# Kernel tuning notes

Measured on AMD Instinct MI355X. Metric: run time of the kernel, lower is better.

Reference implementation:

```python
import jax, jax.numpy as jnp
import numpy as np

NUM_R = 725
NUM_T = 180
EPS = 1e-6


def _hough(img):
    """Discrete Hough transform: params[r, t] = sum of img along line
    x*cos(theta_t) + y*sin(theta_t) = rho_r.
    Gather form: sweep along the longer axis of the line (x-sweep when
    |sin|>=|cos|, else y-sweep) so every line is sampled densely.
    """
    W, H = img.shape  # assume square (W == H) so both sweeps share length
    diag = jnp.sqrt(jnp.asarray(W * W + H * H, dtype=img.dtype))
    thetas = jnp.arange(NUM_T, dtype=img.dtype) * (jnp.pi / NUM_T)      # [T]
    rhos = jnp.linspace(-diag, diag, NUM_R, dtype=img.dtype)            # [R]
    cos_t = jnp.cos(thetas)                                             # [T]
    sin_t = jnp.sin(thetas)                                             # [T]
    n = jnp.arange(W)                                                   # sweep coord [N]
    nf = n.astype(img.dtype)

    rho_b = rhos[:, None, None]          # [R,1,1]
    cos_b = cos_t[None, :, None]         # [1,T,1]
    sin_b = sin_t[None, :, None]
    n_b = nf[None, None, :]              # [1,1,N]

    # --- x-sweep: x = n, y = (rho - x*cos) / sin ---
    sin_safe = jnp.where(jnp.abs(sin_b) < EPS, jnp.asarray(1.0, img.dtype), sin_b)
    y_f = (rho_b - n_b * cos_b) / sin_safe
    y_i = jnp.round(y_f).astype(jnp.int32)                              # [R,T,N]
    valid_x = (y_i >= 0) & (y_i < H)
    vals_x = jnp.where(valid_x,
                       img[n[None, None, :], jnp.clip(y_i, 0, H - 1)],
                       jnp.asarray(0.0, img.dtype))

    # --- y-sweep: y = n, x = (rho - y*sin) / cos ---
    cos_safe = jnp.where(jnp.abs(cos_b) < EPS, jnp.asarray(1.0, img.dtype), cos_b)
    x_f = (rho_b - n_b * sin_b) / cos_safe
    x_i = jnp.round(x_f).astype(jnp.int32)
    valid_y = (x_i >= 0) & (x_i < W)
    vals_y = jnp.where(valid_y,
                       img[jnp.clip(x_i, 0, W - 1), n[None, None, :]],
                       jnp.asarray(0.0, img.dtype))

    use_x = (jnp.abs(sin_t) >= jnp.abs(cos_t))[None, :, None]           # [1,T,1]
    vals = jnp.where(use_x, vals_x, vals_y)
    return jnp.sum(vals, axis=-1)                                        # [R,T]


def setup_inputs() -> dict:
    key = jax.random.key(0)
    img = jax.random.uniform(key, (512, 512), dtype=jnp.float32)
    return {"img": img}


def reference(img):
    return _hough(img)
```

## Files before the change

kernel.cpp:

```cpp
#include <hip/hip_runtime.h>
#include <math.h>

#define W 512
#define H 512
#define NUM_R 725
#define NUM_T 180

__global__ __launch_bounds__(256) void transpose_k(const float* __restrict__ in,
                                                   float* __restrict__ out) {
    __shared__ float tile[32][33];
    const int bx = blockIdx.x * 32, by = blockIdx.y * 32;
    const int tx = threadIdx.x, ty = threadIdx.y;
#pragma unroll
    for (int j = 0; j < 32; j += 8)
        tile[ty + j][tx] = in[(size_t)(by + ty + j) * W + (bx + tx)];
    __syncthreads();
#pragma unroll
    for (int j = 0; j < 32; j += 8)
        out[(size_t)(bx + ty + j) * H + (by + tx)] = tile[tx][ty + j];
}

__global__ __launch_bounds__(256) void hough_k(const float* __restrict__ img,
                                               const float* __restrict__ imgT,
                                               float* __restrict__ out,
                                               int hasT) {
    const int t = blockIdx.x;
    const int r = blockIdx.y * 256 + threadIdx.x;
    const int rc = (r < NUM_R) ? r : (NUM_R - 1);

    const double theta = (double)t * (M_PI / 180.0);
    const double s = sin(theta);
    const double c = cos(theta);
    const bool use_x = fabs(s) >= fabs(c);
    double dd = use_x ? s : c;
    if (fabs(dd) < 1e-6) dd = 1.0;
    const double a   = use_x ? c : s;
    const double inv = 1.0 / dd;
    const double nk2 = -(a * inv);

    const double diag = sqrt(524288.0);
    const double step = (2.0 * diag) / 724.0;
    double rho = (double)rc * step - diag;
    if (rc == NUM_R - 1) rho = diag;

    const double SCALE = 1099511627776.0;
    const long long NK2q = (long long)rint(nk2 * SCALE);
    long long Y = (long long)rint(rho * inv * SCALE) + (1ll << 39);

    float acc = 0.f;

    if (use_x || hasT) {
        const float* __restrict__ base = use_x ? img : imgT;
#pragma unroll 8
        for (int n = 0; n < W; ++n) {
            const int y = (int)(Y >> 40);
            Y += NK2q;
            const int yc = min(max(y, 0), W - 1);
            const float v = base[n * W + yc];
            acc += ((unsigned)y < (unsigned)W) ? v : 0.f;
        }
    } else {
#pragma unroll 4
        for (int n = 0; n < W; ++n) {
            const int y = (int)(Y >> 40);
            Y += NK2q;
            const int yc = min(max(y, 0), W - 1);
            const float v = img[yc * W + n];
            acc += ((unsigned)y < (unsigned)W) ? v : 0.f;
        }
    }

    if (r < NUM_R) out[(size_t)r * NUM_T + t] = acc;
}

extern "C" void kernel_launch(void* const* d_in, const int* in_sizes, int n_in,
                              void* d_out, int out_size, void* d_ws, size_t ws_size,
                              hipStream_t stream) {
    const float* img = (const float*)d_in[0];
    float* out = (float*)d_out;

    const int hasT = (ws_size >= (size_t)W * H * sizeof(float)) ? 1 : 0;
    float* imgT = (float*)d_ws;
    if (hasT) {
        transpose_k<<<dim3(16, 16), dim3(32, 8), 0, stream>>>(img, imgT);
    }

    hough_k<<<dim3(NUM_T, (NUM_R + 255) / 256), dim3(256), 0, stream>>>(
        img, hasT ? imgT : img, out, hasT);
}
```

Baseline: 85.60 us.

## Replace gather Hough with pixel-scatter into shared-memory rho accumulators

Switches from a per-(rho,theta) gather along lines to a scatter formulation. Each block takes one theta and a chunk of image rows, reads pixels coalesced as float2, computes each pixel's rho bin in fixed point, and adds the value into shared-memory accumulators when it lies within the rounding window. The block partials are then atomically added into an output zeroed with memset. This removes the transpose pass and the uncoalesced gathers, but adds shared atomics, a global atomic reduction and an extra memset, and it may not reproduce the reference's rounding and bin membership exactly.

```diff
diff --git a/kernel.cpp b/kernel.cpp
--- a/kernel.cpp
+++ b/kernel.cpp
@@ -5,72 +5,69 @@
 #define H 512
 #define NUM_R 725
 #define NUM_T 180
+#define RCHUNK 64
 
-__global__ __launch_bounds__(256) void transpose_k(const float* __restrict__ in,
-                                                   float* __restrict__ out) {
-    __shared__ float tile[32][33];
-    const int bx = blockIdx.x * 32, by = blockIdx.y * 32;
-    const int tx = threadIdx.x, ty = threadIdx.y;
-#pragma unroll
-    for (int j = 0; j < 32; j += 8)
-        tile[ty + j][tx] = in[(size_t)(by + ty + j) * W + (bx + tx)];
+__global__ __launch_bounds__(256) void hough_scatter_k(const float* __restrict__ img,
+                                                       float* __restrict__ out) {
+    const int t   = blockIdx.x;
+    const int n0  = blockIdx.y * RCHUNK;
+    const int tid = threadIdx.x;
+
+    __shared__ float racc[768];
+
+    racc[tid] = 0.f;
+    racc[tid + 256] = 0.f;
+    racc[tid + 512] = 0.f;
     __syncthreads();
-#pragma unroll
-    for (int j = 0; j < 32; j += 8)
-        out[(size_t)(bx + ty + j) * H + (by + tx)] = tile[tx][ty + j];
-}
-
-__global__ __launch_bounds__(256) void hough_k(const float* __restrict__ img,
-                                               const float* __restrict__ imgT,
-                                               float* __restrict__ out,
-                                               int hasT) {
-    const int t = blockIdx.x;
-    const int r = blockIdx.y * 256 + threadIdx.x;
-    const int rc = (r < NUM_R) ? r : (NUM_R - 1);
 
     const double theta = (double)t * (M_PI / 180.0);
     const double s = sin(theta);
     const double c = cos(theta);
-    const bool use_x = fabs(s) >= fabs(c);
-    double dd = use_x ? s : c;
-    if (fabs(dd) < 1e-6) dd = 1.0;
-    const double a   = use_x ? c : s;
-    const double inv = 1.0 / dd;
-    const double nk2 = -(a * inv);
-
     const double diag = sqrt(524288.0);
     const double step = (2.0 * diag) / 724.0;
-    double rho = (double)rc * step - diag;
-    if (rc == NUM_R - 1) rho = diag;
+    const double inv_step = 1.0 / step;
 
-    const double SCALE = 1099511627776.0;
-    const long long NK2q = (long long)rint(nk2 * SCALE);
-    long long Y = (long long)rint(rho * inv * SCALE) + (1ll << 39);
+    const double cstep = c * inv_step;
+    const double sstep = s * inv_step;
+    const double dstep = diag * inv_step;
 
-    float acc = 0.f;
+    const double SC = 4294967296.0;
+    const long long cq = (long long)rint(cstep * SC);
+    const double hw = fmax(fabs(s), fabs(c)) * 0.5 * inv_step;
+    const unsigned hwq = (unsigned)(hw * SC);
+    const unsigned A = 0x80000000u - hwq;
+    const unsigned B = 2u * hwq;
 
-    if (use_x || hasT) {
-        const float* __restrict__ base = use_x ? img : imgT;
+    const int j0 = 2 * tid;
+    const double colpart1 = (double)j0 * sstep + dstep;
+    const double colpart2 = colpart1 + sstep;
+
+    const double nn = (double)n0;
+    long long u1 = (long long)rint((nn * cstep + colpart1) * SC) + (1ll << 31);
+    long long u2 = (long long)rint((nn * cstep + colpart2) * SC) + (1ll << 31);
+
+    const float2* rowp = (const float2*)(img + (size_t)n0 * W) + tid;
+
 #pragma unroll 8
-        for (int n = 0; n < W; ++n) {
-            const int y = (int)(Y >> 40);
-            Y += NK2q;
-            const int yc = min(max(y, 0), W - 1);
-            const float v = base[n * W + yc];
-            acc += ((unsigned)y < (unsigned)W) ? v : 0.f;
-        }
-    } else {
-#pragma unroll 4
-        for (int n = 0; n < W; ++n) {
-            const int y = (int)(Y >> 40);
-            Y += NK2q;
-            const int yc = min(max(y, 0), W - 1);
-            const float v = img[yc * W + n];
-            acc += ((unsigned)y < (unsigned)W) ? v : 0.f;
-        }
+    for (int j = 0; j < RCHUNK; ++j) {
+        const float2 v = rowp[j * (W / 2)];
+        const unsigned F1 = (unsigned)u1;
+        const unsigned F2 = (unsigned)u2;
+        const int r1 = (int)(u1 >> 32);
+        const int r2 = (int)(u2 >> 32);
+        u1 += cq;
+        u2 += cq;
+        if (F1 - A <= B) atomicAdd(&racc[r1], v.x);
+        if (F2 - A <= B) atomicAdd(&racc[r2], v.y);
     }
 
-    if (r < NUM_R) out[(size_t)r * NUM_T + t] = acc;
+    __syncthreads();
+
+#pragma unroll
+    for (int k = 0; k < 3; ++k) {
+        const int r = tid + 256 * k;
+        if (r < NUM_R) atomicAdd(&out[(size_t)r * NUM_T + t], racc[r]);
+    }
 }
 
 extern "C" void kernel_launch(void* const* d_in, const int* in_sizes, int n_in,
@@ -79,12 +76,7 @@
     const float* img = (const float*)d_in[0];
     float* out = (float*)d_out;
 
-    const int hasT = (ws_size >= (size_t)W * H * sizeof(float)) ? 1 : 0;
-    float* imgT = (float*)d_ws;
-    if (hasT) {
-        transpose_k<<<dim3(16, 16), dim3(32, 8), 0, stream>>>(img, imgT);
-    }
+    hipMemsetAsync(d_out, 0, (size_t)NUM_R * NUM_T * sizeof(float), stream);
 
-    hough_k<<<dim3(NUM_T, (NUM_R + 255) / 256), dim3(256), 0, stream>>>(
-        img, hasT ? imgT : img, out, hasT);
+    hough_scatter_k<<<dim3(NUM_T, H / RCHUNK), dim3(256), 0, stream>>>(img, out);
 }
```

Measured after the change: 179.8 us. 2.1x slower.

## Replace gather Hough with pixel-scatter into shared-memory rho accumulators plus reduction

Applied to the files above, without the earlier changes.

Inverts the transform from a per-(rho,theta) gather to a per-pixel scatter. Each block handles one angle and a chunk of 64 rows, reading rows with coalesced float2 loads and adding each pixel into per-wave shared-memory rho histograms. It then writes partial sums that a separate reduce kernel combines across chunks. This removes the uncoalesced gathers, but adds LDS atomics-free races (per-wave buffers), extra kernel launches, a partial-sum buffer and a rounding scheme that must match the reference's validity and rounding exactly.

```diff
diff --git a/kernel.cpp b/kernel.cpp
--- a/kernel.cpp
+++ b/kernel.cpp
@@ -5,6 +5,11 @@
 #define H 512
 #define NUM_R 725
 #define NUM_T 180
+#define RCHUNK 64
+#define NCHUNK (H / RCHUNK)
+#define RPAD 768
+
+#define WS_FLOATS ((size_t)W * H + (size_t)NCHUNK * NUM_T * RPAD)
 
 __global__ __launch_bounds__(256) void transpose_k(const float* __restrict__ in,
                                                    float* __restrict__ out) {
@@ -20,10 +25,93 @@
         out[(size_t)(bx + ty + j) * H + (by + tx)] = tile[tx][ty + j];
 }
 
-__global__ __launch_bounds__(256) void hough_k(const float* __restrict__ img,
-                                               const float* __restrict__ imgT,
-                                               float* __restrict__ out,
-                                               int hasT) {
+__global__ __launch_bounds__(256) void hough_scatter_k(const float* __restrict__ img,
+                                                       const float* __restrict__ imgT,
+                                                       float* __restrict__ partial) {
+    const int t   = blockIdx.x;
+    const int n0  = blockIdx.y * RCHUNK;
+    const int tid = threadIdx.x;
+    const int wave = tid >> 6;
+
+    __shared__ float racc[4 * RPAD];
+
+    {
+        float4* z = (float4*)racc;
+#pragma unroll
+        for (int k = 0; k < 3; ++k)
+            z[tid + 256 * k] = make_float4(0.f, 0.f, 0.f, 0.f);
+    }
+    __syncthreads();
+
+    const double theta = (double)t * (M_PI / 180.0);
+    const double s = sin(theta);
+    const double c = cos(theta);
+    const bool use_x = fabs(s) >= fabs(c);
+    const double diag = sqrt(524288.0);
+    const double step = (2.0 * diag) / 724.0;
+    const double inv_step = 1.0 / step;
+
+    const double lane_co = (use_x ? s : c) * inv_step;
+    const double loop_co = (use_x ? c : s) * inv_step;
+    const double dstep   = diag * inv_step;
+
+    const double SC = 4294967296.0;
+    const long long lq = (long long)rint(loop_co * SC);
+    const unsigned hwq = (unsigned)(fabs(lane_co) * 0.5 * SC);
+    const unsigned A = 0x80000000u - hwq;
+    const unsigned B = 2u * hwq;
+
+    const int p0 = 2 * tid;
+    const double rowpart = (double)n0 * loop_co + dstep;
+    long long u1 = (long long)rint((rowpart + (double)p0 * lane_co) * SC) + (1ll << 31);
+    long long u2 = (long long)rint((rowpart + (double)(p0 + 1) * lane_co) * SC) + (1ll << 31);
+
+    float* racc_w = racc + wave * RPAD;
+    const float* __restrict__ base = use_x ? img : imgT;
+    const float2* rowp = (const float2*)(base + (size_t)n0 * W) + tid;
+
+#pragma unroll 8
+    for (int j = 0; j < RCHUNK; ++j) {
+        const float2 v = rowp[j * (W / 2)];
+        const unsigned F1 = (unsigned)u1;
+        const unsigned F2 = (unsigned)u2;
+        const int r1 = (int)(u1 >> 32);
+        const int r2 = (int)(u2 >> 32);
+        u1 += lq;
+        u2 += lq;
+        if (F1 - A <= B) racc_w[r1] += v.x;
+        if (F2 - A <= B) racc_w[r2] += v.y;
+    }
+
+    __syncthreads();
+
+    float* dst = partial + ((size_t)blockIdx.y * NUM_T + t) * RPAD;
+#pragma unroll
+    for (int k = 0; k < 3; ++k) {
+        const int r = tid + 256 * k;
+        dst[r] = racc[r] + racc[RPAD + r] + racc[2 * RPAD + r] + racc[3 * RPAD + r];
+    }
+}
+
+__global__ __launch_bounds__(256) void reduce_k(const float* __restrict__ partial,
+                                                float* __restrict__ out) {
+    const int t = blockIdx.x;
+    const int tid = threadIdx.x;
+#pragma unroll
+    for (int k = 0; k < 3; ++k) {
+        const int r = tid + 256 * k;
+        if (r < NUM_R) {
+            float acc = 0.f;
+#pragma unroll
+            for (int ch = 0; ch < NCHUNK; ++ch)
+                acc += partial[((size_t)ch * NUM_T + t) * RPAD + r];
+            out[(size_t)r * NUM_T + t] = acc;
+        }
+    }
+}
+
+__global__ __launch_bounds__(256) void hough_gather_k(const float* __restrict__ img,
+                                                      float* __restrict__ out) {
     const int t = blockIdx.x;
     const int r = blockIdx.y * 256 + threadIdx.x;
     const int rc = (r < NUM_R) ? r : (NUM_R - 1);
@@ -34,10 +122,9 @@
     const bool use_x = fabs(s) >= fabs(c);
     double dd = use_x ? s : c;
     if (fabs(dd) < 1e-6) dd = 1.0;
-    const double a   = use_x ? c : s;
+    const double a = use_x ? c : s;
     const double inv = 1.0 / dd;
     const double nk2 = -(a * inv);
-
     const double diag = sqrt(524288.0);
     const double step = (2.0 * diag) / 724.0;
     double rho = (double)rc * step - diag;
@@ -48,15 +135,12 @@
     long long Y = (long long)rint(rho * inv * SCALE) + (1ll << 39);
 
     float acc = 0.f;
-
-    if (use_x || hasT) {
-        const float* __restrict__ base = use_x ? img : imgT;
+    if (use_x) {
 #pragma unroll 8
         for (int n = 0; n < W; ++n) {
             const int y = (int)(Y >> 40);
             Y += NK2q;
-            const int yc = min(max(y, 0), W - 1);
-            const float v = base[n * W + yc];
+            const float v = img[n * W + min(max(y, 0), W - 1)];
             acc += ((unsigned)y < (unsigned)W) ? v : 0.f;
         }
     } else {
@@ -64,12 +148,10 @@
         for (int n = 0; n < W; ++n) {
             const int y = (int)(Y >> 40);
             Y += NK2q;
-            const int yc = min(max(y, 0), W - 1);
-            const float v = img[yc * W + n];
+            const float v = img[min(max(y, 0), W - 1) * W + n];
             acc += ((unsigned)y < (unsigned)W) ? v : 0.f;
         }
     }
-
     if (r < NUM_R) out[(size_t)r * NUM_T + t] = acc;
 }
 
@@ -79,12 +161,14 @@
     const float* img = (const float*)d_in[0];
     float* out = (float*)d_out;
 
-    const int hasT = (ws_size >= (size_t)W * H * sizeof(float)) ? 1 : 0;
-    float* imgT = (float*)d_ws;
-    if (hasT) {
+    if (ws_size >= WS_FLOATS * sizeof(float)) {
+        float* imgT = (float*)d_ws;
+        float* partial = (float*)d_ws + (size_t)W * H;
+
         transpose_k<<<dim3(16, 16), dim3(32, 8), 0, stream>>>(img, imgT);
+        hough_scatter_k<<<dim3(NUM_T, NCHUNK), dim3(256), 0, stream>>>(img, imgT, partial);
+        reduce_k<<<dim3(NUM_T), dim3(256), 0, stream>>>(partial, out);
+    } else {
+        hough_gather_k<<<dim3(NUM_T, (NUM_R + 255) / 256), dim3(256), 0, stream>>>(img, out);
     }
-
-    hough_k<<<dim3(NUM_T, (NUM_R + 255) / 256), dim3(256), 0, stream>>>(
-        img, hasT ? imgT : img, out, hasT);
 }
```

Result: no change. 85.11 us (-0.6%).
